# Kernel optimization log

Measured on AMD Instinct MI355X. Metric: run time of the kernel, lower is better.

Reference implementation:

```python
import jax, jax.numpy as jnp
import numpy as np

B, P, L = 256, 16, 4
NUM_ENTITY, NUM_NODE = 500000, 512
E, C1, C2 = 128, 512, 256


def setup_inputs() -> dict:
    key = jax.random.key(0)
    ks = jax.random.split(key, 13)
    inp = {
        "start_ids": jax.random.randint(ks[0], (B, P), 0, NUM_ENTITY, dtype=jnp.int32),
        "end_ids": jax.random.randint(ks[1], (B, P), 0, NUM_ENTITY, dtype=jnp.int32),
        "module_ids": jax.random.randint(ks[2], (B, P, L), 0, NUM_NODE, dtype=jnp.int32),
        "counts": jax.random.randint(ks[3], (B, P), 1, 10, dtype=jnp.int32),
        # learned parameters
        "embed": jax.random.normal(ks[4], (NUM_ENTITY, E), dtype=jnp.float32) * 0.02,
        "W": jax.random.normal(ks[5], (NUM_NODE, E, E), dtype=jnp.float32) * (1.0 / np.sqrt(E)),
        "b": jax.random.normal(ks[6], (NUM_NODE, E), dtype=jnp.float32) * 0.01,
        "W1": jax.random.normal(ks[7], (C1, 2 * E), dtype=jnp.float32) * (1.0 / np.sqrt(2 * E)),
        "b1": jnp.zeros((C1,), jnp.float32),
        "W2": jax.random.normal(ks[8], (C2, C1), dtype=jnp.float32) * (1.0 / np.sqrt(C1)),
        "b2": jnp.zeros((C2,), jnp.float32),
        "W3": jax.random.normal(ks[9], (1, C2), dtype=jnp.float32) * (1.0 / np.sqrt(C2)),
        "b3": jnp.zeros((1,), jnp.float32),
    }
    return inp


def reference(start_ids, end_ids, module_ids, counts, embed, W, b, W1, b1, W2, b2, W3, b3):
    # Embed path endpoints: [B, P, E]
    x = embed[start_ids]
    y = embed[end_ids]

    # Apply the same per-node Linear chain to both endpoint embeddings.
    # Scan over the L path steps; gather the step's weight matrices per path.
    def step(carry, mids):  # mids: [B, P]
        x, y = carry
        Wg = W[mids]            # [B, P, E, E] (out, in)
        bg = b[mids]            # [B, P, E]
        x = jnp.einsum('bpi,bpoi->bpo', x, Wg) + bg
        y = jnp.einsum('bpi,bpoi->bpo', y, Wg) + bg
        return (x, y), None

    (x, y), _ = jax.lax.scan(step, (x, y), jnp.transpose(module_ids, (2, 0, 1)))

    feat = jnp.concatenate([x, y], axis=-1)          # [B, P, 2E]
    c = counts.astype(feat.dtype)                    # path multiplicities
    pooled = jnp.einsum('bp,bpf->bf', c, feat) / jnp.sum(c, axis=1, keepdims=True)

    h = jax.nn.relu(pooled @ W1.T + b1)
    h = jax.nn.relu(h @ W2.T + b2)
    out = jax.nn.sigmoid(h @ W3.T + b3)              # [B, 1]
    return out
```

## Files before the change

kernel.cpp:

```cpp
#include <hip/hip_runtime.h>
#include <math.h>

#define BB 256
#define PP 16
#define LL 4
#define EE 128
#define NPATH (BB*PP)
#define NMOD 512
#define CC1 512
#define CC2 256

#define WS_FEAT   0
#define WS_WT     ((size_t)NPATH*2*EE*4)
#define WS_END    (WS_WT + (size_t)NMOD*EE*EE*2)

__device__ __forceinline__ unsigned short f2bf(float f) {
    unsigned u = __float_as_uint(f);
    u = (u + 0x7fffu + ((u >> 16) & 1u)) >> 16;
    return (unsigned short)u;
}
__device__ __forceinline__ float bf2f(unsigned short s) {
    return __uint_as_float(((unsigned)s) << 16);
}

__global__ __launch_bounds__(256) void k_wtrans(
    const float* __restrict__ W, unsigned short* __restrict__ Wt)
{
    const int tid = blockIdx.x*256 + threadIdx.x;
    const int o   = tid & 127;
    const int kc  = (tid >> 7) & 15;
    const int mid = tid >> 11;
    const float* src = W + ((size_t)mid*EE + o)*EE + kc*8;
    const float4 a = *(const float4*)(src);
    const float4 b = *(const float4*)(src + 4);
    uint4 u;
    u.x = (unsigned)f2bf(a.x) | ((unsigned)f2bf(a.y) << 16);
    u.y = (unsigned)f2bf(a.z) | ((unsigned)f2bf(a.w) << 16);
    u.z = (unsigned)f2bf(b.x) | ((unsigned)f2bf(b.y) << 16);
    u.w = (unsigned)f2bf(b.z) | ((unsigned)f2bf(b.w) << 16);
    *(uint4*)(Wt + (size_t)tid*8) = u;
}

template<int USEBF>
__global__ __launch_bounds__(256, 4) void k_chain(
    const int* __restrict__ start_ids, const int* __restrict__ end_ids,
    const int* __restrict__ module_ids, const float* __restrict__ embed,
    const float* __restrict__ W, const unsigned short* __restrict__ Wt,
    const float* __restrict__ bvec, float* __restrict__ feat)
{
    const int t = threadIdx.x;
    const int p = t >> 7;
    const int o = t & 127;
    const int bp = blockIdx.x*2 + p;
    __shared__ float sx[2][2][EE];
    __shared__ float sy[2][2][EE];

    sx[p][0][o] = embed[(size_t)start_ids[bp]*EE + o];
    sy[p][0][o] = embed[(size_t)end_ids[bp]*EE + o];
    __syncthreads();

    int cur = 0;
    for (int l = 0; l < LL; ++l) {
        const int mid = module_ids[bp*LL + l];
        float ax = bvec[(size_t)mid*EE + o];
        float ay = ax;
        if (USEBF) {
            const uint4*  wt  = (const uint4*)(Wt + (size_t)mid*16384);
            const float4* xv4 = (const float4*)sx[p][cur];
            const float4* yv4 = (const float4*)sy[p][cur];
            #pragma unroll 8
            for (int kc = 0; kc < 16; ++kc) {
                const uint4 wv = wt[kc*128 + o];
                const float4 xv0 = xv4[kc*2],   yv0 = yv4[kc*2];
                const float4 xv1 = xv4[kc*2+1], yv1 = yv4[kc*2+1];
                const float w0 = bf2f((unsigned short)(wv.x & 0xffffu));
                const float w1 = bf2f((unsigned short)(wv.x >> 16));
                const float w2 = bf2f((unsigned short)(wv.y & 0xffffu));
                const float w3 = bf2f((unsigned short)(wv.y >> 16));
                const float w4 = bf2f((unsigned short)(wv.z & 0xffffu));
                const float w5 = bf2f((unsigned short)(wv.z >> 16));
                const float w6 = bf2f((unsigned short)(wv.w & 0xffffu));
                const float w7 = bf2f((unsigned short)(wv.w >> 16));
                ax = fmaf(w0, xv0.x, ax); ay = fmaf(w0, yv0.x, ay);
                ax = fmaf(w1, xv0.y, ax); ay = fmaf(w1, yv0.y, ay);
                ax = fmaf(w2, xv0.z, ax); ay = fmaf(w2, yv0.z, ay);
                ax = fmaf(w3, xv0.w, ax); ay = fmaf(w3, yv0.w, ay);
                ax = fmaf(w4, xv1.x, ax); ay = fmaf(w4, yv1.x, ay);
                ax = fmaf(w5, xv1.y, ax); ay = fmaf(w5, yv1.y, ay);
                ax = fmaf(w6, xv1.z, ax); ay = fmaf(w6, yv1.z, ay);
                ax = fmaf(w7, xv1.w, ax); ay = fmaf(w7, yv1.w, ay);
            }
        } else {
            const float4* wr = (const float4*)(W + ((size_t)mid*EE + o)*EE);
            #pragma unroll
            for (int i = 0; i < EE; i += 4) {
                const float4 wv = wr[i >> 2];
                const float4 xv = *(const float4*)&sx[p][cur][i];
                const float4 yv = *(const float4*)&sy[p][cur][i];
                ax = fmaf(wv.x, xv.x, ax); ay = fmaf(wv.x, yv.x, ay);
                ax = fmaf(wv.y, xv.y, ax); ay = fmaf(wv.y, yv.y, ay);
                ax = fmaf(wv.z, xv.z, ax); ay = fmaf(wv.z, yv.z, ay);
                ax = fmaf(wv.w, xv.w, ax); ay = fmaf(wv.w, yv.w, ay);
            }
        }
        sx[p][cur^1][o] = ax;
        sy[p][cur^1][o] = ay;
        __syncthreads();
        cur ^= 1;
    }

    feat[(size_t)bp*(2*EE) + o]      = sx[p][cur][o];
    feat[(size_t)bp*(2*EE) + EE + o] = sy[p][cur][o];
}

__global__ __launch_bounds__(256) void k_mlp(
    const int* __restrict__ counts, const float* __restrict__ state,
    const float* __restrict__ W1, const float* __restrict__ b1,
    const float* __restrict__ W2, const float* __restrict__ b2,
    const float* __restrict__ W3, const float* __restrict__ b3,
    float* __restrict__ out)
{
    const int t = threadIdx.x;
    const int b0 = blockIdx.x * 2;
    __shared__ float pl[2][256];
    __shared__ float h1s[2][CC1];
    __shared__ float h2s[2][CC2];
    __shared__ float red[256];

    #pragma unroll
    for (int r = 0; r < 2; ++r) {
        const int b = b0 + r;
        float acc = 0.f, cs = 0.f;
        #pragma unroll
        for (int p = 0; p < PP; ++p) {
            const float cc = (float)counts[b*PP + p];
            cs += cc;
            acc = fmaf(cc, state[((size_t)(b*PP + p))*256 + t], acc);
        }
        pl[r][t] = acc / cs;
    }
    __syncthreads();

    #pragma unroll
    for (int hh = 0; hh < 2; ++hh) {
        const int col = t + hh*256;
        const float4* w4 = (const float4*)(W1 + (size_t)col*256);
        float a0 = b1[col], a1 = a0;
        for (int q = 0; q < 64; ++q) {
            const float4 wv = w4[q];
            const float4 v0 = ((const float4*)pl[0])[q];
            const float4 v1 = ((const float4*)pl[1])[q];
            a0 = fmaf(wv.x,v0.x, fmaf(wv.y,v0.y, fmaf(wv.z,v0.z, fmaf(wv.w,v0.w, a0))));
            a1 = fmaf(wv.x,v1.x, fmaf(wv.y,v1.y, fmaf(wv.z,v1.z, fmaf(wv.w,v1.w, a1))));
        }
        h1s[0][col] = fmaxf(a0, 0.f);
        h1s[1][col] = fmaxf(a1, 0.f);
    }
    __syncthreads();

    {
        const float4* w4 = (const float4*)(W2 + (size_t)t*512);
        float a0 = b2[t], a1 = a0;
        for (int q = 0; q < 128; ++q) {
            const float4 wv = w4[q];
            const float4 v0 = ((const float4*)h1s[0])[q];
            const float4 v1 = ((const float4*)h1s[1])[q];
            a0 = fmaf(wv.x,v0.x, fmaf(wv.y,v0.y, fmaf(wv.z,v0.z, fmaf(wv.w,v0.w, a0))));
            a1 = fmaf(wv.x,v1.x, fmaf(wv.y,v1.y, fmaf(wv.z,v1.z, fmaf(wv.w,v1.w, a1))));
        }
        h2s[0][t] = fmaxf(a0, 0.f);
        h2s[1][t] = fmaxf(a1, 0.f);
    }
    __syncthreads();

    {
        const int r = t >> 7, k = t & 127;
        red[t] = fmaf(W3[k], h2s[r][k], W3[k+128] * h2s[r][k+128]);
        for (int s = 64; s > 0; s >>= 1) {
            __syncthreads();
            if ((t & 127) < s) red[t] += red[t + s];
        }
        __syncthreads();
        if ((t & 127) == 0)
            out[b0 + r] = 1.f / (1.f + expf(-(red[t] + b3[0])));
    }
}

extern "C" void kernel_launch(void* const* d_in, const int* in_sizes, int n_in,
                              void* d_out, int out_size, void* d_ws, size_t ws_size,
                              hipStream_t stream)
{
    const int*   start_ids  = (const int*)d_in[0];
    const int*   end_ids    = (const int*)d_in[1];
    const int*   module_ids = (const int*)d_in[2];
    const int*   counts     = (const int*)d_in[3];
    const float* embed      = (const float*)d_in[4];
    const float* W          = (const float*)d_in[5];
    const float* bvec       = (const float*)d_in[6];
    const float* W1         = (const float*)d_in[7];
    const float* b1         = (const float*)d_in[8];
    const float* W2         = (const float*)d_in[9];
    const float* b2         = (const float*)d_in[10];
    const float* W3         = (const float*)d_in[11];
    const float* b3         = (const float*)d_in[12];
    float* out  = (float*)d_out;
    char*  ws   = (char*)d_ws;
    float* feat = (float*)(ws + WS_FEAT);

    if (ws_size >= WS_END) {
        unsigned short* Wt = (unsigned short*)(ws + WS_WT);
        k_wtrans<<<4096, 256, 0, stream>>>(W, Wt);
        k_chain<1><<<NPATH/2, 256, 0, stream>>>(start_ids, end_ids, module_ids,
                                                embed, W, Wt, bvec, feat);
    } else {
        k_chain<0><<<NPATH/2, 256, 0, stream>>>(start_ids, end_ids, module_ids,
                                                embed, W, (const unsigned short*)0,
                                                bvec, feat);
    }
    k_mlp<<<BB/2, 256, 0, stream>>>(counts, feat, W1, b1, W2, b2, W3, b3, out);
}
```

Before: 428.1 us.

## Fuse path chain and MLP head into one kernel per batch row

Replaces the separate path-chain kernel and MLP kernel with a single kernel that launches one 512-thread block per batch row. The block runs all 16 paths through the 4 linear steps in shared memory, then pools them and computes the MLP head in place. This removes the intermediate feature buffer round-trip to global memory and one kernel launch. In exchange the grid shrinks from 2048 blocks to 256, which cuts the number of waves available to hide weight-load latency. Each block also re-reads W1 and W2, and since there are now twice as many blocks as before, total MLP weight traffic roughly doubles.

```diff
diff --git a/kernel.cpp b/kernel.cpp
--- a/kernel.cpp
+++ b/kernel.cpp
@@ -10,9 +10,9 @@
 #define CC1 512
 #define CC2 256
 
-#define WS_FEAT   0
-#define WS_WT     ((size_t)NPATH*2*EE*4)
-#define WS_END    (WS_WT + (size_t)NMOD*EE*EE*2)
+#define WS_WT     0
+#define WS_FEAT   ((size_t)NMOD*EE*EE*2)
+#define WS_END    (WS_FEAT + (size_t)NPATH*2*EE*4)
 
 __device__ __forceinline__ unsigned short f2bf(float f) {
     unsigned u = __float_as_uint(f);
@@ -41,33 +41,43 @@
     *(uint4*)(Wt + (size_t)tid*8) = u;
 }
 
-template<int USEBF>
-__global__ __launch_bounds__(256, 4) void k_chain(
+__global__ __launch_bounds__(512) void k_row(
     const int* __restrict__ start_ids, const int* __restrict__ end_ids,
-    const int* __restrict__ module_ids, const float* __restrict__ embed,
-    const float* __restrict__ W, const unsigned short* __restrict__ Wt,
-    const float* __restrict__ bvec, float* __restrict__ feat)
+    const int* __restrict__ module_ids, const int* __restrict__ counts,
+    const float* __restrict__ embed, const unsigned short* __restrict__ Wt,
+    const float* __restrict__ bvec,
+    const float* __restrict__ W1, const float* __restrict__ b1,
+    const float* __restrict__ W2, const float* __restrict__ b2,
+    const float* __restrict__ W3, const float* __restrict__ b3,
+    float* __restrict__ out)
 {
     const int t = threadIdx.x;
-    const int p = t >> 7;
-    const int o = t & 127;
-    const int bp = blockIdx.x*2 + p;
-    __shared__ float sx[2][2][EE];
-    __shared__ float sy[2][2][EE];
-
-    sx[p][0][o] = embed[(size_t)start_ids[bp]*EE + o];
-    sy[p][0][o] = embed[(size_t)end_ids[bp]*EE + o];
-    __syncthreads();
-
+    const int b = blockIdx.x;
+    __shared__ float sx[2][PP][EE];
+    __shared__ float sy[2][PP][EE];
+    __shared__ float pl[256];
+    __shared__ float h1s[CC1];
+    __shared__ float h2p[2][CC2];
+    __shared__ float red[256];
+
+    for (int i = t; i < PP*EE; i += 512) {
+        const int p = i >> 7, o = i & 127;
+        sx[0][p][o] = embed[(size_t)start_ids[b*PP + p]*EE + o];
+        sy[0][p][o] = embed[(size_t)end_ids[b*PP + p]*EE + o];
+    }
+    __syncthreads();
+
+    const int pg = t >> 7, o = t & 127;
     int cur = 0;
     for (int l = 0; l < LL; ++l) {
-        const int mid = module_ids[bp*LL + l];
-        float ax = bvec[(size_t)mid*EE + o];
-        float ay = ax;
-        if (USEBF) {
+        for (int pi = 0; pi < PP; pi += 4) {
+            const int p   = pi + pg;
+            const int mid = module_ids[(b*PP + p)*LL + l];
+            float ax = bvec[(size_t)mid*EE + o];
+            float ay = ax;
             const uint4*  wt  = (const uint4*)(Wt + (size_t)mid*16384);
-            const float4* xv4 = (const float4*)sx[p][cur];
-            const float4* yv4 = (const float4*)sy[p][cur];
+            const float4* xv4 = (const float4*)sx[cur][p];
+            const float4* yv4 = (const float4*)sy[cur][p];
             #pragma unroll 8
             for (int kc = 0; kc < 16; ++kc) {
                 const uint4 wv = wt[kc*128 + o];
@@ -90,18 +100,97 @@
                 ax = fmaf(w6, xv1.z, ax); ay = fmaf(w6, yv1.z, ay);
                 ax = fmaf(w7, xv1.w, ax); ay = fmaf(w7, yv1.w, ay);
             }
-        } else {
-            const float4* wr = (const float4*)(W + ((size_t)mid*EE + o)*EE);
-            #pragma unroll
-            for (int i = 0; i < EE; i += 4) {
-                const float4 wv = wr[i >> 2];
-                const float4 xv = *(const float4*)&sx[p][cur][i];
-                const float4 yv = *(const float4*)&sy[p][cur][i];
-                ax = fmaf(wv.x, xv.x, ax); ay = fmaf(wv.x, yv.x, ay);
-                ax = fmaf(wv.y, xv.y, ax); ay = fmaf(wv.y, yv.y, ay);
-                ax = fmaf(wv.z, xv.z, ax); ay = fmaf(wv.z, yv.z, ay);
-                ax = fmaf(wv.w, xv.w, ax); ay = fmaf(wv.w, yv.w, ay);
-            }
+            sx[cur^1][p][o] = ax;
+            sy[cur^1][p][o] = ay;
+        }
+        __syncthreads();
+        cur ^= 1;
+    }
+
+    if (t < 256) {
+        float acc = 0.f, cs = 0.f;
+        #pragma unroll
+        for (int p = 0; p < PP; ++p) {
+            const float cc = (float)counts[b*PP + p];
+            cs += cc;
+            const float v = (t < 128) ? sx[cur][p][t] : sy[cur][p][t - 128];
+            acc = fmaf(cc, v, acc);
+        }
+        pl[t] = acc / cs;
+    }
+    __syncthreads();
+
+    {
+        const float4* w4 = (const float4*)(W1 + (size_t)t*256);
+        float a = b1[t];
+        for (int q = 0; q < 64; ++q) {
+            const float4 wv = w4[q];
+            const float4 v  = ((const float4*)pl)[q];
+            a = fmaf(wv.x,v.x, fmaf(wv.y,v.y, fmaf(wv.z,v.z, fmaf(wv.w,v.w, a))));
+        }
+        h1s[t] = fmaxf(a, 0.f);
+    }
+    __syncthreads();
+
+    {
+        const int col = t & 255, hf = t >> 8;
+        const float4* w4 = (const float4*)(W2 + (size_t)col*CC1 + hf*256);
+        const float4* v4 = (const float4*)(h1s + hf*256);
+        float a = hf ? 0.f : b2[col];
+        for (int q = 0; q < 64; ++q) {
+            const float4 wv = w4[q];
+            const float4 v  = v4[q];
+            a = fmaf(wv.x,v.x, fmaf(wv.y,v.y, fmaf(wv.z,v.z, fmaf(wv.w,v.w, a))));
+        }
+        h2p[hf][col] = a;
+    }
+    __syncthreads();
+
+    if (t < 256) {
+        const float h2 = fmaxf(h2p[0][t] + h2p[1][t], 0.f);
+        red[t] = W3[t] * h2;
+    }
+    __syncthreads();
+    for (int s = 128; s > 0; s >>= 1) {
+        if (t < s) red[t] += red[t + s];
+        __syncthreads();
+    }
+    if (t == 0) out[b] = 1.f / (1.f + expf(-(red[0] + b3[0])));
+}
+
+template<int USEBF>
+__global__ __launch_bounds__(256, 4) void k_chain(
+    const int* __restrict__ start_ids, const int* __restrict__ end_ids,
+    const int* __restrict__ module_ids, const float* __restrict__ embed,
+    const float* __restrict__ W, const unsigned short* __restrict__ Wt,
+    const float* __restrict__ bvec, float* __restrict__ feat)
+{
+    const int t = threadIdx.x;
+    const int p = t >> 7;
+    const int o = t & 127;
+    const int bp = blockIdx.x*2 + p;
+    __shared__ float sx[2][2][EE];
+    __shared__ float sy[2][2][EE];
+
+    sx[p][0][o] = embed[(size_t)start_ids[bp]*EE + o];
+    sy[p][0][o] = embed[(size_t)end_ids[bp]*EE + o];
+    __syncthreads();
+
+    int cur = 0;
+    for (int l = 0; l < LL; ++l) {
+        const int mid = module_ids[bp*LL + l];
+        float ax = bvec[(size_t)mid*EE + o];
+        float ay = ax;
+        const float4* wr = (const float4*)(W + ((size_t)mid*EE + o)*EE);
+        #pragma unroll
+        for (int i = 0; i < EE; i += 4) {
+            const float4 wv = wr[i >> 2];
+            const float4 xv = *(const float4*)&sx[p][cur][i];
+            const float4 yv = *(const float4*)&sy[p][cur][i];
+            ax = fmaf(wv.x, xv.x, ax); ay = fmaf(wv.x, yv.x, ay);
+            ax = fmaf(wv.y, xv.y, ax); ay = fmaf(wv.y, yv.y, ay);
+            ax = fmaf(wv.z, xv.z, ax); ay = fmaf(wv.z, yv.z, ay);
+            ax = fmaf(wv.w, xv.w, ax); ay = fmaf(wv.w, yv.w, ay);
         }
         sx[p][cur^1][o] = ax;
         sy[p][cur^1][o] = ay;
@@ -205,17 +294,18 @@
     const float* b3         = (const float*)d_in[12];
     float* out  = (float*)d_out;
     char*  ws   = (char*)d_ws;
-    float* feat = (float*)(ws + WS_FEAT);
-
-    if (ws_size >= WS_END) {
+
+    if (ws_size >= (size_t)(NMOD*EE*EE*2)) {
         unsigned short* Wt = (unsigned short*)(ws + WS_WT);
         k_wtrans<<<4096, 256, 0, stream>>>(W, Wt);
-        k_chain<1><<<NPATH/2, 256, 0, stream>>>(start_ids, end_ids, module_ids,
-                                                embed, W, Wt, bvec, feat);
+        k_row<<<BB, 512, 0, stream>>>(start_ids, end_ids, module_ids, counts,
+                                      embed, Wt, bvec, W1, b1, W2, b2, W3, b3,
+                                      out);
     } else {
+        float* feat = (float*)ws;
         k_chain<0><<<NPATH/2, 256, 0, stream>>>(start_ids, end_ids, module_ids,
                                                 embed, W, (const unsigned short*)0,
                                                 bvec, feat);
-    }
-    k_mlp<<<BB/2, 256, 0, stream>>>(counts, feat, W1, b1, W2, b2, W3, b3, out);
-}
+        k_mlp<<<BB/2, 256, 0, stream>>>(counts, feat, W1, b1, W2, b2, W3, b3, out);
+    }
+}
```

Result: slower. 439.3 us (+2.6%).
